# Kernel tuning notes

Measured on AMD Instinct MI355X. Metric: run time of the kernel, lower is better.

The kernel has to match this reference:

```python
import jax, jax.numpy as jnp
import numpy as np


def _gcn_conv(h, src, dst, W, b, n):
    # PyG GCNConv: x @ W, then symmetric-normalized aggregation with self-loops
    deg = jax.ops.segment_sum(jnp.ones(src.shape[0], h.dtype), dst, num_segments=n)
    dinv = jax.lax.rsqrt(jnp.maximum(deg, 1.0))  # deg >= 1 because self-loops are included
    norm = dinv[src] * dinv[dst]                 # [E]
    m = (h @ W)[src] * norm[:, None]             # gather + scale
    return jax.ops.segment_sum(m, dst, num_segments=n) + b


def setup_inputs() -> dict:
    key = jax.random.key(0)
    N, E, F, H, L, V = 50000, 800000, 128, 256, 64, 128
    ks = jax.random.split(key, 16)
    s = lambda fan_in: 1.0 / np.sqrt(fan_in)
    return {
        "x": jax.random.randint(ks[0], (N,), 0, V),
        "edge_index": jax.random.randint(ks[1], (2, E), 0, N),
        "eps": jax.random.normal(ks[2], (N, L), jnp.float32),
        "emb": jax.random.normal(ks[3], (V, F), jnp.float32),
        "W1": jax.random.normal(ks[4], (F, H), jnp.float32) * s(F),
        "b1": jnp.zeros((H,), jnp.float32),
        "W2": jax.random.normal(ks[5], (H, H), jnp.float32) * s(H),
        "b2": jnp.zeros((H,), jnp.float32),
        "Wmu": jax.random.normal(ks[6], (H, L), jnp.float32) * s(H),
        "bmu": jnp.zeros((L,), jnp.float32),
        "Wlv": jax.random.normal(ks[7], (H, L), jnp.float32) * s(H),
        "blv": jnp.zeros((L,), jnp.float32),
        "W3": jax.random.normal(ks[8], (L, H), jnp.float32) * s(L),
        "b3": jnp.zeros((H,), jnp.float32),
        "W4": jax.random.normal(ks[9], (H, V), jnp.float32) * s(H),
        "b4": jnp.zeros((V,), jnp.float32),
        "Wcap": jax.random.normal(ks[10], (L, 1), jnp.float32) * s(L),
        "bcap": jnp.zeros((1,), jnp.float32),
    }


def reference(x, edge_index, eps, emb, W1, b1, W2, b2, Wmu, bmu, Wlv, blv, W3, b3, W4, b4, Wcap, bcap):
    n = x.shape[0]
    loops = jnp.arange(n, dtype=edge_index.dtype)
    src = jnp.concatenate([edge_index[0], loops])  # add self-loops once, reuse
    dst = jnp.concatenate([edge_index[1], loops])

    h = emb[x]                                      # [N, F] embedding lookup
    h = jax.nn.relu(_gcn_conv(h, src, dst, W1, b1, n))
    h = jax.nn.relu(_gcn_conv(h, src, dst, W2, b2, n))
    mu = h @ Wmu + bmu
    logvar = h @ Wlv + blv
    z = mu + eps * jnp.exp(0.5 * logvar)            # reparameterize
    recon_x = jax.nn.relu(z @ W3 + b3) @ W4 + b4    # decode
    capitalize = jax.nn.sigmoid(z @ Wcap + bcap)
    return recon_x, capitalize, mu, logvar
```

## Files before the change

kernel.cpp:

```cpp
#include <hip/hip_runtime.h>
#include <math.h>


typedef __attribute__((ext_vector_type(8))) short bf16x8;
typedef __attribute__((ext_vector_type(4))) float f32x4;

__device__ inline unsigned short f2bf(float x) {
    unsigned u = __float_as_uint(x);
    return (unsigned short)((u + 0x7FFFu + ((u >> 16) & 1u)) >> 16);
}
__device__ inline float bf2f(unsigned short h) {
    return __uint_as_float(((unsigned)h) << 16);
}

__global__ __launch_bounds__(256) void k_init(int* __restrict__ degint,
                                              int* __restrict__ cursor, int N) {
    int i = blockIdx.x * 256 + threadIdx.x;
    if (i < N) { degint[i] = 1; cursor[i] = 0; }
}

__global__ __launch_bounds__(256) void k_deg_count(const int* __restrict__ dst,
                                                   int* __restrict__ degint, int E) {
    int e = blockIdx.x * 256 + threadIdx.x;
    if (e < E) atomicAdd(&degint[dst[e]], 1);
}

__global__ __launch_bounds__(256) void k_dinv(const int* __restrict__ degint,
                                              float* __restrict__ dinv, int N) {
    int i = blockIdx.x * 256 + threadIdx.x;
    if (i < N) dinv[i] = rsqrtf((float)degint[i]);
}

#define SCAN_BLOCK 1024
__global__ __launch_bounds__(SCAN_BLOCK) void k_scan_local(
        const int* __restrict__ degint, int* __restrict__ row_ptr,
        int* __restrict__ bsum, int N) {
    __shared__ int s[SCAN_BLOCK];
    int gid = blockIdx.x * SCAN_BLOCK + threadIdx.x;
    int v = (gid < N) ? (degint[gid] - 1) : 0;
    s[threadIdx.x] = v;
    __syncthreads();
    for (int off = 1; off < SCAN_BLOCK; off <<= 1) {
        int t = (threadIdx.x >= off) ? s[threadIdx.x - off] : 0;
        __syncthreads();
        s[threadIdx.x] += t;
        __syncthreads();
    }
    if (gid < N) row_ptr[gid] = s[threadIdx.x] - v;
    if (threadIdx.x == SCAN_BLOCK - 1) bsum[blockIdx.x] = s[SCAN_BLOCK - 1];
}

__global__ void k_scan_bsum(int* __restrict__ bsum, int nb) {
    if (blockIdx.x == 0 && threadIdx.x == 0) {
        int acc = 0;
        for (int i = 0; i < nb; ++i) { int v = bsum[i]; bsum[i] = acc; acc += v; }
    }
}

__global__ __launch_bounds__(256) void k_scan_add(int* __restrict__ row_ptr,
                                                  const int* __restrict__ bsum,
                                                  int N, int E) {
    int gid = blockIdx.x * 256 + threadIdx.x;
    if (gid < N) row_ptr[gid] += bsum[gid / SCAN_BLOCK];
    if (gid == 0) row_ptr[N] = E;
}

__global__ __launch_bounds__(256) void k_csr_fill(
        const int* __restrict__ src, const int* __restrict__ dst,
        const int* __restrict__ row_ptr, int* __restrict__ cursor,
        int* __restrict__ csr_src, int E) {
    int e = blockIdx.x * 256 + threadIdx.x;
    if (e < E) {
        int d = dst[e];
        int pos = atomicAdd(&cursor[d], 1);
        csr_src[row_ptr[d] + pos] = src[e];
    }
}

__global__ __launch_bounds__(256) void k_cvtB(
        const float* __restrict__ B, unsigned short* __restrict__ Bth,
        unsigned short* __restrict__ Btl, int K, int Ncol) {
    int i = blockIdx.x * 256 + threadIdx.x;
    if (i >= K * Ncol) return;
    int k = i / Ncol, n = i - k * Ncol;
    float v = B[i];
    unsigned short h = f2bf(v);
    Bth[(long)n * K + k] = h;
    Btl[(long)n * K + k] = f2bf(v - bf2f(h));
}

__global__ __launch_bounds__(256) void k_cvt_tab(
        const float* __restrict__ src, unsigned short* __restrict__ dst, int n) {
    int i = blockIdx.x * 256 + threadIdx.x;
    if (i < n) dst[i] = f2bf(src[i]);
}

__global__ __launch_bounds__(256) void k_gemm_f32(
        const float* __restrict__ A, const float* __restrict__ B,
        float* __restrict__ C, int M, int K, int Ncol) {
    constexpr int BM = 64, BN = 64, BK = 16;
    __shared__ float As[BK][BM];
    __shared__ float Bs[BK][BN];
    const int tid = threadIdx.x;
    const int tx = tid & 15, ty = tid >> 4;
    const int rowBase = blockIdx.x * BM;
    const int colBase = blockIdx.y * BN;
    const int lr = tid >> 2, lc4 = tid & 3;
    const int br = tid >> 4, bc4 = tid & 15;
    const int arow = rowBase + lr;
    const int K4 = K >> 2, N4 = Ncol >> 2;
    const float4* A4 = (const float4*)A;
    const float4* B4 = (const float4*)B;
    float acc[4][4] = {{0.f}};
    for (int k0 = 0; k0 < K; k0 += BK) {
        float4 av = make_float4(0.f, 0.f, 0.f, 0.f);
        if (arow < M) av = A4[(long)arow * K4 + (k0 >> 2) + lc4];
        As[lc4 * 4 + 0][lr] = av.x;
        As[lc4 * 4 + 1][lr] = av.y;
        As[lc4 * 4 + 2][lr] = av.z;
        As[lc4 * 4 + 3][lr] = av.w;
        float4 bv = B4[(long)(k0 + br) * N4 + (colBase >> 2) + bc4];
        *(float4*)&Bs[br][bc4 * 4] = bv;
        __syncthreads();
#pragma unroll
        for (int k = 0; k < BK; ++k) {
            float4 a4v = *(const float4*)&As[k][ty * 4];
            float4 b4v = *(const float4*)&Bs[k][tx * 4];
            float aa[4] = {a4v.x, a4v.y, a4v.z, a4v.w};
            float bb[4] = {b4v.x, b4v.y, b4v.z, b4v.w};
#pragma unroll
            for (int i = 0; i < 4; ++i)
#pragma unroll
                for (int j = 0; j < 4; ++j)
                    acc[i][j] = fmaf(aa[i], bb[j], acc[i][j]);
        }
        __syncthreads();
    }
#pragma unroll
    for (int i = 0; i < 4; ++i) {
        int row = rowBase + ty * 4 + i;
        if (row < M) {
            float4 o = make_float4(acc[i][0], acc[i][1], acc[i][2], acc[i][3]);
            ((float4*)C)[(long)row * N4 + (colBase >> 2) + tx] = o;
        }
    }
}

template<bool RELU, bool BIAS, bool OUTBF>
__global__ __launch_bounds__(256) void k_gemm_mfma(
        const unsigned short* __restrict__ A,
        const unsigned short* __restrict__ Bth, const unsigned short* __restrict__ Btl,
        const float* __restrict__ bias, float* __restrict__ Cf,
        unsigned short* __restrict__ Cb, int M, int K, int Ncol) {
    __shared__ unsigned short Ash[128][40];
    __shared__ unsigned short Bsh[64][40];
    __shared__ unsigned short Bsl[64][40];
    const int tid = threadIdx.x;
    const int lane = tid & 63, w = tid >> 6;
    const int fr = lane & 15, quad = lane >> 4;
    const int wm0 = w * 32;
    const int rowBase = blockIdx.x * 128;
    const int colBase = blockIdx.y * 64;

    const int arow = tid >> 1;
    const int ahalf = (tid & 1) << 4;
    int agrow = rowBase + arow; if (agrow >= M) agrow = M - 1;
    const long abase = (long)agrow * K + ahalf;
    const int bt = tid & 127;
    const int brow = bt >> 1;
    const int bhalf = (bt & 1) << 4;
    const long bbase = (long)(colBase + brow) * K + bhalf;
    const unsigned short* Bsrc = (tid < 128) ? Bth : Btl;
    unsigned short* Bdst = (tid < 128) ? &Bsh[brow][bhalf] : &Bsl[brow][bhalf];

    f32x4 acc[2][4];
#pragma unroll
    for (int i = 0; i < 2; ++i)
#pragma unroll
        for (int j = 0; j < 4; ++j) acc[i][j] = (f32x4){0.f, 0.f, 0.f, 0.f};

    for (int k0 = 0; k0 < K; k0 += 32) {
        *(bf16x8*)&Ash[arow][ahalf]     = *(const bf16x8*)&A[abase + k0];
        *(bf16x8*)&Ash[arow][ahalf + 8] = *(const bf16x8*)&A[abase + k0 + 8];
        *(bf16x8*)Bdst       = *(const bf16x8*)&Bsrc[bbase + k0];
        *(bf16x8*)(Bdst + 8) = *(const bf16x8*)&Bsrc[bbase + k0 + 8];
        __syncthreads();
        bf16x8 ahf[2], bhf[4], blf[4];
#pragma unroll
        for (int i = 0; i < 2; ++i)
            ahf[i] = *(const bf16x8*)&Ash[wm0 + i * 16 + fr][quad * 8];
#pragma unroll
        for (int j = 0; j < 4; ++j) {
            bhf[j] = *(const bf16x8*)&Bsh[j * 16 + fr][quad * 8];
            blf[j] = *(const bf16x8*)&Bsl[j * 16 + fr][quad * 8];
        }
#pragma unroll
        for (int i = 0; i < 2; ++i)
#pragma unroll
            for (int j = 0; j < 4; ++j) {
                acc[i][j] = __builtin_amdgcn_mfma_f32_16x16x32_bf16(
                    ahf[i], bhf[j], acc[i][j], 0, 0, 0);
                acc[i][j] = __builtin_amdgcn_mfma_f32_16x16x32_bf16(
                    ahf[i], blf[j], acc[i][j], 0, 0, 0);
            }
        __syncthreads();
    }

#pragma unroll
    for (int i = 0; i < 2; ++i) {
        const int rowb = rowBase + wm0 + i * 16 + quad * 4;
#pragma unroll
        for (int j = 0; j < 4; ++j) {
            const int col = colBase + j * 16 + fr;
            const float bv = BIAS ? bias[col] : 0.f;
#pragma unroll
            for (int r = 0; r < 4; ++r) {
                const int row = rowb + r;
                if (row < M) {
                    float v = acc[i][j][r] + bv;
                    if (RELU) v = fmaxf(v, 0.f);
                    const long o = (long)row * Ncol + col;
                    if (OUTBF) Cb[o] = f2bf(v);
                    else       Cf[o] = v;
                }
            }
        }
    }
}

__global__ __launch_bounds__(256) void k_gemm_heads(
        const unsigned short* __restrict__ A,
        const unsigned short* __restrict__ Bth, const unsigned short* __restrict__ Btl,
        const float* __restrict__ bmu, const float* __restrict__ blv,
        const float* __restrict__ eps, const float* __restrict__ Wcap,
        const float* __restrict__ bcap, float* __restrict__ mu,
        float* __restrict__ lv, unsigned short* __restrict__ Zh,
        float* __restrict__ cap, int M) {
    constexpr int K = 256;
    __shared__ unsigned short Ash[64][40];
    __shared__ unsigned short Bsh[128][40];
    __shared__ unsigned short Bsl[128][40];
    const int tid = threadIdx.x;
    const int lane = tid & 63, w = tid >> 6;
    const int fr = lane & 15, quad = lane >> 4;
    const int wm0 = w * 16;
    const int rowBase = blockIdx.x * 64;

    const int arow = tid >> 2;
    const int aseg = (tid & 3) << 3;
    int agrow = rowBase + arow; if (agrow >= M) agrow = M - 1;
    const long abase = (long)agrow * K + aseg;
    const int brow = tid >> 1;
    const int bseg = (tid & 1) << 4;
    const long bbase = (long)brow * K + bseg;

    f32x4 acc[8];
#pragma unroll
    for (int j = 0; j < 8; ++j) acc[j] = (f32x4){0.f, 0.f, 0.f, 0.f};

    for (int k0 = 0; k0 < K; k0 += 32) {
        *(bf16x8*)&Ash[arow][aseg] = *(const bf16x8*)&A[abase + k0];
        *(bf16x8*)&Bsh[brow][bseg]     = *(const bf16x8*)&Bth[bbase + k0];
        *(bf16x8*)&Bsh[brow][bseg + 8] = *(const bf16x8*)&Bth[bbase + k0 + 8];
        *(bf16x8*)&Bsl[brow][bseg]     = *(const bf16x8*)&Btl[bbase + k0];
        *(bf16x8*)&Bsl[brow][bseg + 8] = *(const bf16x8*)&Btl[bbase + k0 + 8];
        __syncthreads();
        bf16x8 ahf = *(const bf16x8*)&Ash[wm0 + fr][quad * 8];
#pragma unroll
        for (int j = 0; j < 8; ++j) {
            bf16x8 bhf = *(const bf16x8*)&Bsh[j * 16 + fr][quad * 8];
            bf16x8 blf = *(const bf16x8*)&Bsl[j * 16 + fr][quad * 8];
            acc[j] = __builtin_amdgcn_mfma_f32_16x16x32_bf16(ahf, bhf, acc[j], 0, 0, 0);
            acc[j] = __builtin_amdgcn_mfma_f32_16x16x32_bf16(ahf, blf, acc[j], 0, 0, 0);
        }
        __syncthreads();
    }

    float capacc[4] = {0.f, 0.f, 0.f, 0.f};
#pragma unroll
    for (int j = 0; j < 4; ++j) {
        const int c = j * 16 + fr;
        const float bm = bmu[c], bl = blv[c];
        const float wc = Wcap[c];
#pragma unroll
        for (int r = 0; r < 4; ++r) {
            const int row = rowBase + wm0 + quad * 4 + r;
            if (row < M) {
                const long o = (long)row * 64 + c;
                float mv = acc[j][r] + bm;
                float lvv = acc[j + 4][r] + bl;
                mu[o] = mv;
                lv[o] = lvv;
                float zz = fmaf(eps[o], expf(0.5f * lvv), mv);
                Zh[o] = f2bf(zz);
                capacc[r] = fmaf(zz, wc, capacc[r]);
            }
        }
    }
    const float b0 = bcap[0];
#pragma unroll
    for (int r = 0; r < 4; ++r) {
        float v = capacc[r];
        v += __shfl_xor(v, 1, 64);
        v += __shfl_xor(v, 2, 64);
        v += __shfl_xor(v, 4, 64);
        v += __shfl_xor(v, 8, 64);
        if (fr == 0) {
            const int row = rowBase + wm0 + quad * 4 + r;
            if (row < M) cap[row] = 1.f / (1.f + expf(-(v + b0)));
        }
    }
}

__global__ __launch_bounds__(256) void k_agg_tab(
        const unsigned short* __restrict__ tab, const int* __restrict__ x,
        const int* __restrict__ row_ptr, const int* __restrict__ csr_src,
        const float* __restrict__ dinv, const float* __restrict__ bias,
        unsigned short* __restrict__ h1, int N) {
    const int wave = threadIdx.x >> 6;
    const int lane = threadIdx.x & 63;
    const int node = blockIdx.x * 4 + wave;
    if (node >= N) return;
    const ushort4* t4 = (const ushort4*)tab;
    const float di = dinv[node];
    const float selfw = di * di;
    ushort4 a = t4[(long)x[node] * 64 + lane];
    float ax = bf2f(a.x) * selfw, ay = bf2f(a.y) * selfw;
    float az = bf2f(a.z) * selfw, aw = bf2f(a.w) * selfw;
    const int beg = row_ptr[node], end = row_ptr[node + 1];
    for (int e = beg; e < end; ++e) {
        int s = csr_src[e];
        float wgt = dinv[s] * di;
        ushort4 v = t4[(long)x[s] * 64 + lane];
        ax = fmaf(bf2f(v.x), wgt, ax); ay = fmaf(bf2f(v.y), wgt, ay);
        az = fmaf(bf2f(v.z), wgt, az); aw = fmaf(bf2f(v.w), wgt, aw);
    }
    float4 b = ((const float4*)bias)[lane];
    ax = fmaxf(ax + b.x, 0.f); ay = fmaxf(ay + b.y, 0.f);
    az = fmaxf(az + b.z, 0.f); aw = fmaxf(aw + b.w, 0.f);
    ushort4 o;
    o.x = f2bf(ax); o.y = f2bf(ay); o.z = f2bf(az); o.w = f2bf(aw);
    ((ushort4*)h1)[(long)node * 64 + lane] = o;
}

__global__ __launch_bounds__(256) void k_agg_nb(
        const unsigned short* __restrict__ h1, const int* __restrict__ row_ptr,
        const int* __restrict__ csr_src, const float* __restrict__ dinv,
        unsigned short* __restrict__ Ob, int N) {
    const int wave = threadIdx.x >> 6;
    const int lane = threadIdx.x & 63;
    const int node = blockIdx.x * 4 + wave;
    if (node >= N) return;
    const ushort4* h4 = (const ushort4*)h1;
    const float di = dinv[node];
    const float selfw = di * di;
    ushort4 a = h4[(long)node * 64 + lane];
    float ax = bf2f(a.x) * selfw, ay = bf2f(a.y) * selfw;
    float az = bf2f(a.z) * selfw, aw = bf2f(a.w) * selfw;
    const int beg = row_ptr[node], end = row_ptr[node + 1];
    int e = beg;
    for (; e + 1 < end; e += 2) {
        int s0 = csr_src[e], s1 = csr_src[e + 1];
        float w0 = dinv[s0] * di, w1 = dinv[s1] * di;
        ushort4 v0 = h4[(long)s0 * 64 + lane];
        ushort4 v1 = h4[(long)s1 * 64 + lane];
        ax = fmaf(bf2f(v0.x), w0, ax); ay = fmaf(bf2f(v0.y), w0, ay);
        az = fmaf(bf2f(v0.z), w0, az); aw = fmaf(bf2f(v0.w), w0, aw);
        ax = fmaf(bf2f(v1.x), w1, ax); ay = fmaf(bf2f(v1.y), w1, ay);
        az = fmaf(bf2f(v1.z), w1, az); aw = fmaf(bf2f(v1.w), w1, aw);
    }
    if (e < end) {
        int s = csr_src[e];
        float wgt = dinv[s] * di;
        ushort4 v = h4[(long)s * 64 + lane];
        ax = fmaf(bf2f(v.x), wgt, ax); ay = fmaf(bf2f(v.y), wgt, ay);
        az = fmaf(bf2f(v.z), wgt, az); aw = fmaf(bf2f(v.w), wgt, aw);
    }
    ushort4 o;
    o.x = f2bf(ax); o.y = f2bf(ay); o.z = f2bf(az); o.w = f2bf(aw);
    ((ushort4*)Ob)[(long)node * 64 + lane] = o;
}

extern "C" void kernel_launch(void* const* d_in, const int* in_sizes, int n_in,
                              void* d_out, int out_size, void* d_ws, size_t ws_size,
                              hipStream_t stream) {
    const int*   x    = (const int*)d_in[0];
    const int*   ei   = (const int*)d_in[1];
    const float* eps  = (const float*)d_in[2];
    const float* emb  = (const float*)d_in[3];
    const float* W1   = (const float*)d_in[4];
    const float* b1   = (const float*)d_in[5];
    const float* W2   = (const float*)d_in[6];
    const float* b2   = (const float*)d_in[7];
    const float* Wmu  = (const float*)d_in[8];
    const float* bmu  = (const float*)d_in[9];
    const float* Wlv  = (const float*)d_in[10];
    const float* blv  = (const float*)d_in[11];
    const float* W3   = (const float*)d_in[12];
    const float* b3   = (const float*)d_in[13];
    const float* W4   = (const float*)d_in[14];
    const float* b4   = (const float*)d_in[15];
    const float* Wcap = (const float*)d_in[16];
    const float* bcap = (const float*)d_in[17];

    const int N = in_sizes[0];
    const int E = in_sizes[1] / 2;
    const int H = in_sizes[5];
    const int L = in_sizes[9];
    const int V = in_sizes[15];
    const int F = in_sizes[4] / H;

    const int* src = ei;
    const int* dst = ei + E;

    char* w = (char*)d_ws;
    unsigned short* h1b  = (unsigned short*)w; w += (size_t)N * H * 2;
    unsigned short* a2b  = (unsigned short*)w; w += (size_t)N * H * 2;
    unsigned short* h2b  = (unsigned short*)w; w += (size_t)N * H * 2;
    unsigned short* zh   = (unsigned short*)w; w += (size_t)N * L * 2;
    int*   degint = (int*)w;   w += (size_t)N * 4;
    int*   rowp   = (int*)w;   w += (size_t)(N + 1) * 4;
    int*   cursor = (int*)w;   w += (size_t)N * 4;
    float* dinv   = (float*)w; w += (size_t)N * 4;
    int*   bsum   = (int*)w;   w += 256 * 4;
    int*   csrsrc = (int*)w;   w += (size_t)E * 4;
    float* embW1  = (float*)w; w += (size_t)V * H * 4;
    unsigned short* tabH  = (unsigned short*)w; w += (size_t)V * H * 2;
    unsigned short* W2th  = (unsigned short*)w; w += (size_t)H * H * 2;
    unsigned short* W2tl  = (unsigned short*)w; w += (size_t)H * H * 2;
    unsigned short* Wmlth = (unsigned short*)w; w += (size_t)H * 2 * L * 2;
    unsigned short* Wmltl = (unsigned short*)w; w += (size_t)H * 2 * L * 2;
    unsigned short* W3th  = (unsigned short*)w; w += (size_t)L * H * 2;
    unsigned short* W3tl  = (unsigned short*)w; w += (size_t)L * H * 2;
    unsigned short* W4th  = (unsigned short*)w; w += (size_t)H * V * 2;
    unsigned short* W4tl  = (unsigned short*)w; w += (size_t)H * V * 2;

    unsigned short* tb = a2b;

    float* outp    = (float*)d_out;
    float* recon   = outp;
    float* cap     = outp + (size_t)N * V;
    float* mu      = outp + (size_t)N * V + N;
    float* logvar  = mu + (size_t)N * L;

    const int nN  = (N + 255) / 256;
    const int nE  = (E + 255) / 256;
    const int nSc = (N + SCAN_BLOCK - 1) / SCAN_BLOCK;
    const int gM128 = (N + 127) / 128;
    const int gM64  = (N + 63) / 64;

    k_init<<<nN, 256, 0, stream>>>(degint, cursor, N);
    k_deg_count<<<nE, 256, 0, stream>>>(dst, degint, E);
    k_dinv<<<nN, 256, 0, stream>>>(degint, dinv, N);
    k_scan_local<<<nSc, SCAN_BLOCK, 0, stream>>>(degint, rowp, bsum, N);
    k_scan_bsum<<<1, 64, 0, stream>>>(bsum, nSc);
    k_scan_add<<<nN, 256, 0, stream>>>(rowp, bsum, N, E);
    k_csr_fill<<<nE, 256, 0, stream>>>(src, dst, rowp, cursor, csrsrc, E);

    k_cvtB<<<(H * H + 255) / 256, 256, 0, stream>>>(W2, W2th, W2tl, H, H);
    k_cvtB<<<(H * L + 255) / 256, 256, 0, stream>>>(Wmu, Wmlth, Wmltl, H, L);
    k_cvtB<<<(H * L + 255) / 256, 256, 0, stream>>>(
        Wlv, Wmlth + (size_t)L * H, Wmltl + (size_t)L * H, H, L);
    k_cvtB<<<(L * H + 255) / 256, 256, 0, stream>>>(W3, W3th, W3tl, L, H);
    k_cvtB<<<(H * V + 255) / 256, 256, 0, stream>>>(W4, W4th, W4tl, H, V);

    k_gemm_f32<<<dim3(V / 64, H / 64), 256, 0, stream>>>(emb, W1, embW1, V, F, H);
    k_cvt_tab<<<(V * H + 255) / 256, 256, 0, stream>>>(embW1, tabH, V * H);
    k_agg_tab<<<(N + 3) / 4, 256, 0, stream>>>(
        tabH, x, rowp, csrsrc, dinv, b1, h1b, N);

    k_agg_nb<<<(N + 3) / 4, 256, 0, stream>>>(h1b, rowp, csrsrc, dinv, a2b, N);
    k_gemm_mfma<true, true, true><<<dim3(gM128, H / 64), 256, 0, stream>>>(
        a2b, W2th, W2tl, b2, nullptr, h2b, N, H, H);

    k_gemm_heads<<<gM64, 256, 0, stream>>>(
        h2b, Wmlth, Wmltl, bmu, blv, eps, Wcap, bcap, mu, logvar, zh, cap, N);

    k_gemm_mfma<true, true, true><<<dim3(gM128, H / 64), 256, 0, stream>>>(
        zh, W3th, W3tl, b3, nullptr, tb, N, L, H);
    k_gemm_mfma<false, true, false><<<dim3(gM128, V / 64), 256, 0, stream>>>(
        tb, W4th, W4tl, b4, recon, nullptr, N, H, V);
}
```

Before: 469.7 us.

## Precompute edge weights into packed CSR and fuse small setup kernels

Builds the CSR with self-loops included and packs a precomputed normalization weight next to each source index (and next to the embedding id for layer 1). Both aggregation kernels then drop their per-edge dinv and x lookups and unroll by four. It also folds dinv into the scan, merges the five weight-conversion launches into one, and writes the embedding table straight to bf16 from the GEMM. In exchange the packed arrays double index storage, and the CSR fill does extra random dinv and x reads.

```diff
diff --git a/kernel.cpp b/kernel.cpp
--- a/kernel.cpp
+++ b/kernel.cpp
@@ -25,20 +25,15 @@
     if (e < E) atomicAdd(&degint[dst[e]], 1);
 }
 
-__global__ __launch_bounds__(256) void k_dinv(const int* __restrict__ degint,
-                                              float* __restrict__ dinv, int N) {
-    int i = blockIdx.x * 256 + threadIdx.x;
-    if (i < N) dinv[i] = rsqrtf((float)degint[i]);
-}
-
 #define SCAN_BLOCK 1024
 __global__ __launch_bounds__(SCAN_BLOCK) void k_scan_local(
         const int* __restrict__ degint, int* __restrict__ row_ptr,
-        int* __restrict__ bsum, int N) {
+        int* __restrict__ bsum, float* __restrict__ dinv, int N) {
     __shared__ int s[SCAN_BLOCK];
     int gid = blockIdx.x * SCAN_BLOCK + threadIdx.x;
-    int v = (gid < N) ? (degint[gid] - 1) : 0;
-    s[threadIdx.x] = v;
+    int d = (gid < N) ? degint[gid] : 0;
+    if (gid < N) dinv[gid] = rsqrtf((float)d);
+    s[threadIdx.x] = d;
     __syncthreads();
     for (int off = 1; off < SCAN_BLOCK; off <<= 1) {
         int t = (threadIdx.x >= off) ? s[threadIdx.x - off] : 0;
@@ -46,7 +41,7 @@
         s[threadIdx.x] += t;
         __syncthreads();
     }
-    if (gid < N) row_ptr[gid] = s[threadIdx.x] - v;
+    if (gid < N) row_ptr[gid] = s[threadIdx.x] - d;
     if (threadIdx.x == SCAN_BLOCK - 1) bsum[blockIdx.x] = s[SCAN_BLOCK - 1];
 }
 
@@ -59,45 +54,74 @@
 
 __global__ __launch_bounds__(256) void k_scan_add(int* __restrict__ row_ptr,
                                                   const int* __restrict__ bsum,
-                                                  int N, int E) {
+                                                  int N, int T) {
     int gid = blockIdx.x * 256 + threadIdx.x;
     if (gid < N) row_ptr[gid] += bsum[gid / SCAN_BLOCK];
-    if (gid == 0) row_ptr[N] = E;
+    if (gid == 0) row_ptr[N] = T;
 }
 
 __global__ __launch_bounds__(256) void k_csr_fill(
         const int* __restrict__ src, const int* __restrict__ dst,
+        const int* __restrict__ x, const float* __restrict__ dinv,
         const int* __restrict__ row_ptr, int* __restrict__ cursor,
-        int* __restrict__ csr_src, int E) {
+        int2* __restrict__ packA, int2* __restrict__ packB, int E) {
     int e = blockIdx.x * 256 + threadIdx.x;
     if (e < E) {
-        int d = dst[e];
-        int pos = atomicAdd(&cursor[d], 1);
-        csr_src[row_ptr[d] + pos] = src[e];
-    }
-}
-
-__global__ __launch_bounds__(256) void k_cvtB(
-        const float* __restrict__ B, unsigned short* __restrict__ Bth,
-        unsigned short* __restrict__ Btl, int K, int Ncol) {
+        int s = src[e], d = dst[e];
+        float w = dinv[s] * dinv[d];
+        int pos = row_ptr[d] + atomicAdd(&cursor[d], 1);
+        packA[pos] = make_int2(__float_as_int(w), x[s]);
+        packB[pos] = make_int2(__float_as_int(w), s);
+    }
+}
+
+__global__ __launch_bounds__(256) void k_self_fill(
+        const int* __restrict__ x, const float* __restrict__ dinv,
+        const int* __restrict__ row_ptr, int* __restrict__ cursor,
+        int2* __restrict__ packA, int2* __restrict__ packB, int N) {
+    int i = blockIdx.x * 256 + threadIdx.x;
+    if (i < N) {
+        float di = dinv[i];
+        float w = di * di;
+        int pos = row_ptr[i] + atomicAdd(&cursor[i], 1);
+        packA[pos] = make_int2(__float_as_int(w), x[i]);
+        packB[pos] = make_int2(__float_as_int(w), i);
+    }
+}
+
+__global__ __launch_bounds__(256) void k_cvt_all(
+        const float* __restrict__ B0, unsigned short* __restrict__ h0,
+        unsigned short* __restrict__ l0, int K0, int N0,
+        const float* __restrict__ B1, unsigned short* __restrict__ h1,
+        unsigned short* __restrict__ l1, int K1, int N1,
+        const float* __restrict__ B2, unsigned short* __restrict__ h2,
+        unsigned short* __restrict__ l2, int K2, int N2,
+        const float* __restrict__ B3, unsigned short* __restrict__ h3,
+        unsigned short* __restrict__ l3, int K3, int N3,
+        const float* __restrict__ B4, unsigned short* __restrict__ h4,
+        unsigned short* __restrict__ l4, int K4, int N4) {
+    const float* B; unsigned short *Bh, *Bl; int K, Ncol;
+    switch (blockIdx.y) {
+        case 0: B = B0; Bh = h0; Bl = l0; K = K0; Ncol = N0; break;
+        case 1: B = B1; Bh = h1; Bl = l1; K = K1; Ncol = N1; break;
+        case 2: B = B2; Bh = h2; Bl = l2; K = K2; Ncol = N2; break;
+        case 3: B = B3; Bh = h3; Bl = l3; K = K3; Ncol = N3; break;
+        default: B = B4; Bh = h4; Bl = l4; K = K4; Ncol = N4; break;
+    }
     int i = blockIdx.x * 256 + threadIdx.x;
     if (i >= K * Ncol) return;
     int k = i / Ncol, n = i - k * Ncol;
     float v = B[i];
     unsigned short h = f2bf(v);
-    Bth[(long)n * K + k] = h;
-    Btl[(long)n * K + k] = f2bf(v - bf2f(h));
-}
-
-__global__ __launch_bounds__(256) void k_cvt_tab(
-        const float* __restrict__ src, unsigned short* __restrict__ dst, int n) {
-    int i = blockIdx.x * 256 + threadIdx.x;
-    if (i < n) dst[i] = f2bf(src[i]);
-}
-
+    Bh[(long)n * K + k] = h;
+    Bl[(long)n * K + k] = f2bf(v - bf2f(h));
+}
+
+template<bool OUTBF>
 __global__ __launch_bounds__(256) void k_gemm_f32(
         const float* __restrict__ A, const float* __restrict__ B,
-        float* __restrict__ C, int M, int K, int Ncol) {
+        float* __restrict__ C, unsigned short* __restrict__ Cb,
+        int M, int K, int Ncol) {
     constexpr int BM = 64, BN = 64, BK = 16;
     __shared__ float As[BK][BM];
     __shared__ float Bs[BK][BN];
@@ -140,8 +164,15 @@
     for (int i = 0; i < 4; ++i) {
         int row = rowBase + ty * 4 + i;
         if (row < M) {
-            float4 o = make_float4(acc[i][0], acc[i][1], acc[i][2], acc[i][3]);
-            ((float4*)C)[(long)row * N4 + (colBase >> 2) + tx] = o;
+            if (OUTBF) {
+                ushort4 o;
+                o.x = f2bf(acc[i][0]); o.y = f2bf(acc[i][1]);
+                o.z = f2bf(acc[i][2]); o.w = f2bf(acc[i][3]);
+                *(ushort4*)&Cb[(long)row * Ncol + colBase + tx * 4] = o;
+            } else {
+                float4 o = make_float4(acc[i][0], acc[i][1], acc[i][2], acc[i][3]);
+                ((float4*)C)[(long)row * N4 + (colBase >> 2) + tx] = o;
+            }
         }
     }
 }
@@ -313,27 +344,40 @@
 }
 
 __global__ __launch_bounds__(256) void k_agg_tab(
-        const unsigned short* __restrict__ tab, const int* __restrict__ x,
-        const int* __restrict__ row_ptr, const int* __restrict__ csr_src,
-        const float* __restrict__ dinv, const float* __restrict__ bias,
+        const unsigned short* __restrict__ tab, const int* __restrict__ row_ptr,
+        const int2* __restrict__ packA, const float* __restrict__ bias,
         unsigned short* __restrict__ h1, int N) {
     const int wave = threadIdx.x >> 6;
     const int lane = threadIdx.x & 63;
     const int node = blockIdx.x * 4 + wave;
     if (node >= N) return;
     const ushort4* t4 = (const ushort4*)tab;
-    const float di = dinv[node];
-    const float selfw = di * di;
-    ushort4 a = t4[(long)x[node] * 64 + lane];
-    float ax = bf2f(a.x) * selfw, ay = bf2f(a.y) * selfw;
-    float az = bf2f(a.z) * selfw, aw = bf2f(a.w) * selfw;
+    float ax = 0.f, ay = 0.f, az = 0.f, aw = 0.f;
     const int beg = row_ptr[node], end = row_ptr[node + 1];
-    for (int e = beg; e < end; ++e) {
-        int s = csr_src[e];
-        float wgt = dinv[s] * di;
-        ushort4 v = t4[(long)x[s] * 64 + lane];
-        ax = fmaf(bf2f(v.x), wgt, ax); ay = fmaf(bf2f(v.y), wgt, ay);
-        az = fmaf(bf2f(v.z), wgt, az); aw = fmaf(bf2f(v.w), wgt, aw);
+    int e = beg;
+    for (; e + 4 <= end; e += 4) {
+        int2 p0 = packA[e], p1 = packA[e + 1], p2 = packA[e + 2], p3 = packA[e + 3];
+        ushort4 v0 = t4[(long)p0.y * 64 + lane];
+        ushort4 v1 = t4[(long)p1.y * 64 + lane];
+        ushort4 v2 = t4[(long)p2.y * 64 + lane];
+        ushort4 v3 = t4[(long)p3.y * 64 + lane];
+        float w0 = __int_as_float(p0.x), w1 = __int_as_float(p1.x);
+        float w2 = __int_as_float(p2.x), w3 = __int_as_float(p3.x);
+        ax = fmaf(bf2f(v0.x), w0, ax); ay = fmaf(bf2f(v0.y), w0, ay);
+        az = fmaf(bf2f(v0.z), w0, az); aw = fmaf(bf2f(v0.w), w0, aw);
+        ax = fmaf(bf2f(v1.x), w1, ax); ay = fmaf(bf2f(v1.y), w1, ay);
+        az = fmaf(bf2f(v1.z), w1, az); aw = fmaf(bf2f(v1.w), w1, aw);
+        ax = fmaf(bf2f(v2.x), w2, ax); ay = fmaf(bf2f(v2.y), w2, ay);
+        az = fmaf(bf2f(v2.z), w2, az); aw = fmaf(bf2f(v2.w), w2, aw);
+        ax = fmaf(bf2f(v3.x), w3, ax); ay = fmaf(bf2f(v3.y), w3, ay);
+        az = fmaf(bf2f(v3.z), w3, az); aw = fmaf(bf2f(v3.w), w3, aw);
+    }
+    for (; e < end; ++e) {
+        int2 p = packA[e];
+        float w0 = __int_as_float(p.x);
+        ushort4 v = t4[(long)p.y * 64 + lane];
+        ax = fmaf(bf2f(v.x), w0, ax); ay = fmaf(bf2f(v.y), w0, ay);
+        az = fmaf(bf2f(v.z), w0, az); aw = fmaf(bf2f(v.w), w0, aw);
     }
     float4 b = ((const float4*)bias)[lane];
     ax = fmaxf(ax + b.x, 0.f); ay = fmaxf(ay + b.y, 0.f);
@@ -345,36 +389,38 @@
 
 __global__ __launch_bounds__(256) void k_agg_nb(
         const unsigned short* __restrict__ h1, const int* __restrict__ row_ptr,
-        const int* __restrict__ csr_src, const float* __restrict__ dinv,
-        unsigned short* __restrict__ Ob, int N) {
+        const int2* __restrict__ packB, unsigned short* __restrict__ Ob, int N) {
     const int wave = threadIdx.x >> 6;
     const int lane = threadIdx.x & 63;
     const int node = blockIdx.x * 4 + wave;
     if (node >= N) return;
     const ushort4* h4 = (const ushort4*)h1;
-    const float di = dinv[node];
-    const float selfw = di * di;
-    ushort4 a = h4[(long)node * 64 + lane];
-    float ax = bf2f(a.x) * selfw, ay = bf2f(a.y) * selfw;
-    float az = bf2f(a.z) * selfw, aw = bf2f(a.w) * selfw;
+    float ax = 0.f, ay = 0.f, az = 0.f, aw = 0.f;
     const int beg = row_ptr[node], end = row_ptr[node + 1];
     int e = beg;
-    for (; e + 1 < end; e += 2) {
-        int s0 = csr_src[e], s1 = csr_src[e + 1];
-        float w0 = dinv[s0] * di, w1 = dinv[s1] * di;
-        ushort4 v0 = h4[(long)s0 * 64 + lane];
-        ushort4 v1 = h4[(long)s1 * 64 + lane];
+    for (; e + 4 <= end; e += 4) {
+        int2 p0 = packB[e], p1 = packB[e + 1], p2 = packB[e + 2], p3 = packB[e + 3];
+        ushort4 v0 = h4[(long)p0.y * 64 + lane];
+        ushort4 v1 = h4[(long)p1.y * 64 + lane];
+        ushort4 v2 = h4[(long)p2.y * 64 + lane];
+        ushort4 v3 = h4[(long)p3.y * 64 + lane];
+        float w0 = __int_as_float(p0.x), w1 = __int_as_float(p1.x);
+        float w2 = __int_as_float(p2.x), w3 = __int_as_float(p3.x);
         ax = fmaf(bf2f(v0.x), w0, ax); ay = fmaf(bf2f(v0.y), w0, ay);
         az = fmaf(bf2f(v0.z), w0, az); aw = fmaf(bf2f(v0.w), w0, aw);
         ax = fmaf(bf2f(v1.x), w1, ax); ay = fmaf(bf2f(v1.y), w1, ay);
         az = fmaf(bf2f(v1.z), w1, az); aw = fmaf(bf2f(v1.w), w1, aw);
-    }
-    if (e < end) {
-        int s = csr_src[e];
-        float wgt = dinv[s] * di;
-        ushort4 v = h4[(long)s * 64 + lane];
-        ax = fmaf(bf2f(v.x), wgt, ax); ay = fmaf(bf2f(v.y), wgt, ay);
-        az = fmaf(bf2f(v.z), wgt, az); aw = fmaf(bf2f(v.w), wgt, aw);
+        ax = fmaf(bf2f(v2.x), w2, ax); ay = fmaf(bf2f(v2.y), w2, ay);
+        az = fmaf(bf2f(v2.z), w2, az); aw = fmaf(bf2f(v2.w), w2, aw);
+        ax = fmaf(bf2f(v3.x), w3, ax); ay = fmaf(bf2f(v3.y), w3, ay);
+        az = fmaf(bf2f(v3.z), w3, az); aw = fmaf(bf2f(v3.w), w3, aw);
+    }
+    for (; e < end; ++e) {
+        int2 p = packB[e];
+        float w0 = __int_as_float(p.x);
+        ushort4 v = h4[(long)p.y * 64 + lane];
+        ax = fmaf(bf2f(v.x), w0, ax); ay = fmaf(bf2f(v.y), w0, ay);
+        az = fmaf(bf2f(v.z), w0, az); aw = fmaf(bf2f(v.w), w0, aw);
     }
     ushort4 o;
     o.x = f2bf(ax); o.y = f2bf(ay); o.z = f2bf(az); o.w = f2bf(aw);
@@ -409,6 +455,7 @@
     const int L = in_sizes[9];
     const int V = in_sizes[15];
     const int F = in_sizes[4] / H;
+    const int T = E + N;
 
     const int* src = ei;
     const int* dst = ei + E;
@@ -423,8 +470,8 @@
     int*   cursor = (int*)w;   w += (size_t)N * 4;
     float* dinv   = (float*)w; w += (size_t)N * 4;
     int*   bsum   = (int*)w;   w += 256 * 4;
-    int*   csrsrc = (int*)w;   w += (size_t)E * 4;
-    float* embW1  = (float*)w; w += (size_t)V * H * 4;
+    int2*  packA  = (int2*)w;  w += (size_t)T * 8;
+    int2*  packB  = (int2*)w;  w += (size_t)T * 8;
     unsigned short* tabH  = (unsigned short*)w; w += (size_t)V * H * 2;
     unsigned short* W2th  = (unsigned short*)w; w += (size_t)H * H * 2;
     unsigned short* W2tl  = (unsigned short*)w; w += (size_t)H * H * 2;
@@ -451,25 +498,25 @@
 
     k_init<<<nN, 256, 0, stream>>>(degint, cursor, N);
     k_deg_count<<<nE, 256, 0, stream>>>(dst, degint, E);
-    k_dinv<<<nN, 256, 0, stream>>>(degint, dinv, N);
-    k_scan_local<<<nSc, SCAN_BLOCK, 0, stream>>>(degint, rowp, bsum, N);
+    k_scan_local<<<nSc, SCAN_BLOCK, 0, stream>>>(degint, rowp, bsum, dinv, N);
     k_scan_bsum<<<1, 64, 0, stream>>>(bsum, nSc);
-    k_scan_add<<<nN, 256, 0, stream>>>(rowp, bsum, N, E);
-    k_csr_fill<<<nE, 256, 0, stream>>>(src, dst, rowp, cursor, csrsrc, E);
-
-    k_cvtB<<<(H * H + 255) / 256, 256, 0, stream>>>(W2, W2th, W2tl, H, H);
-    k_cvtB<<<(H * L + 255) / 256, 256, 0, stream>>>(Wmu, Wmlth, Wmltl, H, L);
-    k_cvtB<<<(H * L + 255) / 256, 256, 0, stream>>>(
-        Wlv, Wmlth + (size_t)L * H, Wmltl + (size_t)L * H, H, L);
-    k_cvtB<<<(L * H + 255) / 256, 256, 0, stream>>>(W3, W3th, W3tl, L, H);
-    k_cvtB<<<(H * V + 255) / 256, 256, 0, stream>>>(W4, W4th, W4tl, H, V);
-
-    k_gemm_f32<<<dim3(V / 64, H / 64), 256, 0, stream>>>(emb, W1, embW1, V, F, H);
-    k_cvt_tab<<<(V * H + 255) / 256, 256, 0, stream>>>(embW1, tabH, V * H);
-    k_agg_tab<<<(N + 3) / 4, 256, 0, stream>>>(
-        tabH, x, rowp, csrsrc, dinv, b1, h1b, N);
-
-    k_agg_nb<<<(N + 3) / 4, 256, 0, stream>>>(h1b, rowp, csrsrc, dinv, a2b, N);
+    k_scan_add<<<nN, 256, 0, stream>>>(rowp, bsum, N, T);
+    k_csr_fill<<<nE, 256, 0, stream>>>(src, dst, x, dinv, rowp, cursor,
+                                       packA, packB, E);
+    k_self_fill<<<nN, 256, 0, stream>>>(x, dinv, rowp, cursor, packA, packB, N);
+
+    k_cvt_all<<<dim3((H * H + 255) / 256, 5), 256, 0, stream>>>(
+        W2, W2th, W2tl, H, H,
+        Wmu, Wmlth, Wmltl, H, L,
+        Wlv, Wmlth + (size_t)L * H, Wmltl + (size_t)L * H, H, L,
+        W3, W3th, W3tl, L, H,
+        W4, W4th, W4tl, H, V);
+
+    k_gemm_f32<true><<<dim3(V / 64, H / 64), 256, 0, stream>>>(
+        emb, W1, nullptr, tabH, V, F, H);
+    k_agg_tab<<<(N + 3) / 4, 256, 0, stream>>>(tabH, rowp, packA, b1, h1b, N);
+
+    k_agg_nb<<<(N + 3) / 4, 256, 0, stream>>>(h1b, rowp, packB, a2b, N);
     k_gemm_mfma<true, true, true><<<dim3(gM128, H / 64), 256, 0, stream>>>(
         a2b, W2th, W2tl, b2, nullptr, h2b, N, H, H);
 
```

New measurement: 428.2 us. 1.1x faster.
